# Performance work log

Measured on AMD Instinct MI355X. Metric: run time of the kernel, lower is better.

## Reference

```python
import jax, jax.numpy as jnp
import numpy as np

D_MODEL = 1024
N_HEADS = 16
HEAD_DIM = D_MODEL // N_HEADS
BATCH = 4
SEQ = 2048


def setup_inputs() -> dict:
    key = jax.random.key(0)
    ks = jax.random.split(key, 5)
    # Xavier uniform bound for square d_model x d_model weights
    bound = np.sqrt(6.0 / (D_MODEL + D_MODEL))
    x = jax.random.normal(ks[0], (BATCH, SEQ, D_MODEL), dtype=jnp.float32)
    attention_mask = jnp.ones((BATCH, SEQ), dtype=jnp.int32)
    wq = jax.random.uniform(ks[1], (D_MODEL, D_MODEL), jnp.float32, -bound, bound)
    wk = jax.random.uniform(ks[2], (D_MODEL, D_MODEL), jnp.float32, -bound, bound)
    wv = jax.random.uniform(ks[3], (D_MODEL, D_MODEL), jnp.float32, -bound, bound)
    wo = jax.random.uniform(ks[4], (D_MODEL, D_MODEL), jnp.float32, -bound, bound)
    return {"x": x, "attention_mask": attention_mask,
            "wq": wq, "wk": wk, "wv": wv, "wo": wo}


def reference(x, attention_mask, wq, wk, wv, wo):
    # x: (B, S, D). Linear weights stored torch-style (out, in): y = x @ W^T
    B, S, D = x.shape
    H, Hd = N_HEADS, HEAD_DIM
    scale = np.sqrt(Hd).astype(np.float32)

    def split_heads(t):  # (B,S,D) -> (B,H,S,Hd)
        return t.reshape(B, S, H, Hd).transpose(0, 2, 1, 3)

    q = split_heads(jnp.einsum('bsd,ed->bse', x, wq))
    k = split_heads(jnp.einsum('bsd,ed->bse', x, wk))
    v = split_heads(jnp.einsum('bsd,ed->bse', x, wv))

    scores = jnp.einsum('bhqd,bhkd->bhqk', q, k) / scale  # (B,H,S,S)

    causal = jnp.tril(jnp.ones((S, S), dtype=bool))  # True = keep
    keep = causal[None, None, :, :] & (attention_mask[:, None, None, :] != 0)
    scores = jnp.where(keep, scores, -jnp.inf)

    attn = jax.nn.softmax(scores, axis=-1)  # dropout: eval mode (identity)
    out = jnp.einsum('bhqk,bhkd->bhqd', attn, v)  # (B,H,S,Hd)
    out = out.transpose(0, 2, 1, 3).reshape(B, S, D)
    return jnp.einsum('bsd,ed->bse', out, wo)
```

## Files before the change

kernel.cpp:

```cpp
#include <hip/hip_runtime.h>
#include <cstdint>
#include <cstddef>

#define D_MODEL 1024
#define N_HEADS 16
#define HEAD_DIM 64
#define BATCH 4
#define SEQ 2048
#define M_TOTAL (BATCH * SEQ)

typedef __attribute__((ext_vector_type(8))) short bf16x8;
typedef __attribute__((ext_vector_type(4))) float f32x4;
typedef __attribute__((ext_vector_type(16))) float f32x16;

#define Q_SCALE 0.18033688011112042f

__device__ __forceinline__ unsigned short f2bu(float f) {
    union { float f; unsigned u; } x; x.f = f;
    unsigned r = x.u + 0x7FFFu + ((x.u >> 16) & 1u);
    return (unsigned short)(r >> 16);
}

__device__ __forceinline__ void async16(void* lds, const void* g) {
    __builtin_amdgcn_global_load_lds(
        (const __attribute__((address_space(1))) void*)g,
        (__attribute__((address_space(3))) void*)lds, 16, 0, 0);
}

__global__ __launch_bounds__(256) void cast_all(const float* __restrict__ x,
                                                const float* __restrict__ wq,
                                                const float* __restrict__ wk,
                                                const float* __restrict__ wv,
                                                const float* __restrict__ wo,
                                                unsigned short* __restrict__ dst) {
    const size_t NE = (size_t)M_TOTAL * D_MODEL;
    const size_t WE = (size_t)D_MODEL * D_MODEL;
    size_t i4 = (size_t)blockIdx.x * 256 + threadIdx.x;
    size_t e = i4 * 4;
    const float* src; size_t off;
    if (e < NE) { src = x; off = e; }
    else {
        size_t t = e - NE;
        int r = (int)(t / WE); off = t - (size_t)r * WE;
        src = (r == 0) ? wq : (r == 1) ? wk : (r == 2) ? wv : wo;
    }
    float4 v = *(const float4*)(src + off);
    ushort4 o;
    o.x = f2bu(v.x); o.y = f2bu(v.y); o.z = f2bu(v.z); o.w = f2bu(v.w);
    ((ushort4*)dst)[i4] = o;
}

__global__ __launch_bounds__(256) void qkv_gemm(const unsigned short* __restrict__ X,
                                                const unsigned short* __restrict__ W0,
                                                const unsigned short* __restrict__ W1,
                                                const unsigned short* __restrict__ W2,
                                                unsigned short* __restrict__ Y0,
                                                unsigned short* __restrict__ Y1,
                                                unsigned short* __restrict__ Vt) {
    __shared__ short As[2][128 * 32];
    __shared__ short Bs[2][128 * 32];

    const int id = (int)blockIdx.x + 24 * (int)blockIdx.y;
    const int xcd = id & 7, slot = id >> 3;
    const int ty = xcd * 8 + slot / 24;
    const int tx = slot % 24;

    const int sel = tx >> 3;
    const unsigned short* W = (sel == 0) ? W0 : (sel == 1) ? W1 : W2;
    const float scl = (sel == 0) ? Q_SCALE : 1.0f;

    const int tid = threadIdx.x;
    const int w = tid >> 6, lane = tid & 63, quad = lane >> 4, l15 = lane & 15;
    const int wm = w & 1, wn = w >> 1;
    const int rowBase = ty * 128;
    const int colBase = (tx & 7) * 128;

    int stRow[2], stCc[2];
#pragma unroll
    for (int l = 0; l < 2; ++l) {
        int c = tid + l * 256;
        stRow[l] = c >> 2;
        stCc[l] = (c & 3) ^ ((stRow[l] >> 1) & 3);
    }

    f32x4 acc[4][4];
#pragma unroll
    for (int mi = 0; mi < 4; ++mi)
#pragma unroll
        for (int ni = 0; ni < 4; ++ni)
#pragma unroll
            for (int e = 0; e < 4; ++e) acc[mi][ni][e] = 0.f;

#pragma unroll
    for (int l = 0; l < 2; ++l) {
        int c = tid + l * 256;
        async16((char*)As[0] + c * 16, X + (size_t)(rowBase + stRow[l]) * 1024 + stCc[l] * 8);
        async16((char*)Bs[0] + c * 16, W + (size_t)(colBase + stRow[l]) * 1024 + stCc[l] * 8);
    }
    __syncthreads();

    for (int kt = 0; kt < 32; ++kt) {
        const int buf = kt & 1;
        if (kt < 31) {
            const int kn = (kt + 1) * 32;
#pragma unroll
            for (int l = 0; l < 2; ++l) {
                int c = tid + l * 256;
                async16((char*)As[buf ^ 1] + c * 16,
                        X + (size_t)(rowBase + stRow[l]) * 1024 + kn + stCc[l] * 8);
                async16((char*)Bs[buf ^ 1] + c * 16,
                        W + (size_t)(colBase + stRow[l]) * 1024 + kn + stCc[l] * 8);
            }
        }

        bf16x8 a[4], b[4];
#pragma unroll
        for (int mi = 0; mi < 4; ++mi) {
            int r = wm * 64 + mi * 16 + l15;
            int slt = quad ^ ((r >> 1) & 3);
            a[mi] = *(const bf16x8*)&As[buf][r * 32 + slt * 8];
        }
#pragma unroll
        for (int ni = 0; ni < 4; ++ni) {
            int r = wn * 64 + ni * 16 + l15;
            int slt = quad ^ ((r >> 1) & 3);
            b[ni] = *(const bf16x8*)&Bs[buf][r * 32 + slt * 8];
        }
#pragma unroll
        for (int mi = 0; mi < 4; ++mi)
#pragma unroll
            for (int ni = 0; ni < 4; ++ni)
                acc[mi][ni] = __builtin_amdgcn_mfma_f32_16x16x32_bf16(a[mi], b[ni], acc[mi][ni], 0, 0, 0);

        __syncthreads();
    }

    if (sel != 2) {
        unsigned short* Y = (sel == 0) ? Y0 : Y1;
#pragma unroll
        for (int mi = 0; mi < 4; ++mi)
#pragma unroll
            for (int ni = 0; ni < 4; ++ni)
#pragma unroll
                for (int reg = 0; reg < 4; ++reg) {
                    int row = rowBase + wm * 64 + mi * 16 + quad * 4 + reg;
                    int col = colBase + wn * 64 + ni * 16 + l15;
                    Y[(size_t)row * 1024 + col] = f2bu(acc[mi][ni][reg] * scl);
                }
    } else {
#pragma unroll
        for (int mi = 0; mi < 4; ++mi) {
            int row0 = rowBase + wm * 64 + mi * 16 + quad * 4;
            int bb = row0 >> 11;
            int s0 = row0 & 2047;
#pragma unroll
            for (int ni = 0; ni < 4; ++ni) {
                int col = colBase + wn * 64 + ni * 16 + l15;
                int hh = col >> 6, dd = col & 63;
                ushort4 pk;
                pk.x = f2bu(acc[mi][ni][0]); pk.y = f2bu(acc[mi][ni][1]);
                pk.z = f2bu(acc[mi][ni][2]); pk.w = f2bu(acc[mi][ni][3]);
                *(ushort4*)(Vt + (((size_t)bb * 16 + hh) * 64 + dd) * SEQ + s0) = pk;
            }
        }
    }
}

__global__ __launch_bounds__(256) void out_gemm(const unsigned short* __restrict__ X,
                                                const unsigned short* __restrict__ W,
                                                float* __restrict__ Y) {
    __shared__ short As[2][128 * 32];
    __shared__ short Bs[2][128 * 32];

    const int id = (int)blockIdx.x + 8 * (int)blockIdx.y;
    const int xcd = id & 7, slot = id >> 3;
    const int ty = xcd * 8 + (slot >> 3);
    const int tx = slot & 7;

    const int tid = threadIdx.x;
    const int w = tid >> 6, lane = tid & 63, quad = lane >> 4, l15 = lane & 15;
    const int wm = w & 1, wn = w >> 1;
    const int rowBase = ty * 128;
    const int colBase = tx * 128;

    int stRow[2], stCc[2];
#pragma unroll
    for (int l = 0; l < 2; ++l) {
        int c = tid + l * 256;
        stRow[l] = c >> 2;
        stCc[l] = (c & 3) ^ ((stRow[l] >> 1) & 3);
    }

    f32x4 acc[4][4];
#pragma unroll
    for (int mi = 0; mi < 4; ++mi)
#pragma unroll
        for (int ni = 0; ni < 4; ++ni)
#pragma unroll
            for (int e = 0; e < 4; ++e) acc[mi][ni][e] = 0.f;

#pragma unroll
    for (int l = 0; l < 2; ++l) {
        int c = tid + l * 256;
        async16((char*)As[0] + c * 16, X + (size_t)(rowBase + stRow[l]) * 1024 + stCc[l] * 8);
        async16((char*)Bs[0] + c * 16, W + (size_t)(colBase + stRow[l]) * 1024 + stCc[l] * 8);
    }
    __syncthreads();

    for (int kt = 0; kt < 32; ++kt) {
        const int buf = kt & 1;
        if (kt < 31) {
            const int kn = (kt + 1) * 32;
#pragma unroll
            for (int l = 0; l < 2; ++l) {
                int c = tid + l * 256;
                async16((char*)As[buf ^ 1] + c * 16,
                        X + (size_t)(rowBase + stRow[l]) * 1024 + kn + stCc[l] * 8);
                async16((char*)Bs[buf ^ 1] + c * 16,
                        W + (size_t)(colBase + stRow[l]) * 1024 + kn + stCc[l] * 8);
            }
        }

        bf16x8 a[4], b[4];
#pragma unroll
        for (int mi = 0; mi < 4; ++mi) {
            int r = wm * 64 + mi * 16 + l15;
            int slt = quad ^ ((r >> 1) & 3);
            a[mi] = *(const bf16x8*)&As[buf][r * 32 + slt * 8];
        }
#pragma unroll
        for (int ni = 0; ni < 4; ++ni) {
            int r = wn * 64 + ni * 16 + l15;
            int slt = quad ^ ((r >> 1) & 3);
            b[ni] = *(const bf16x8*)&Bs[buf][r * 32 + slt * 8];
        }
#pragma unroll
        for (int mi = 0; mi < 4; ++mi)
#pragma unroll
            for (int ni = 0; ni < 4; ++ni)
                acc[mi][ni] = __builtin_amdgcn_mfma_f32_16x16x32_bf16(a[mi], b[ni], acc[mi][ni], 0, 0, 0);

        __syncthreads();
    }

#pragma unroll
    for (int mi = 0; mi < 4; ++mi)
#pragma unroll
        for (int ni = 0; ni < 4; ++ni)
#pragma unroll
            for (int reg = 0; reg < 4; ++reg) {
                int row = rowBase + wm * 64 + mi * 16 + quad * 4 + reg;
                int col = colBase + wn * 64 + ni * 16 + l15;
                Y[(size_t)row * 1024 + col] = acc[mi][ni][reg];
            }
}

__global__ __launch_bounds__(256) void flash32(const unsigned short* __restrict__ Q,
                                               const unsigned short* __restrict__ K,
                                               const unsigned short* __restrict__ Vt,
                                               const int* __restrict__ mask,
                                               unsigned short* __restrict__ CTX) {
    __shared__ short lds[16384];
    __shared__ float biasS[2][64];
    __shared__ int allokS[2];
    __shared__ int okW[4];

    const int bh = blockIdx.x;
    const int pid = blockIdx.y;
    const int b = bh >> 4;
    const int tid = threadIdx.x;
    const int w = tid >> 6, lane = tid & 63, l31 = lane & 31, lane5 = lane >> 5;

    const size_t qkBase = (size_t)b * SEQ * D_MODEL + (size_t)(bh & 15) * HEAD_DIM;
    const size_t vtBase = (size_t)bh * HEAD_DIM * SEQ;

    {
        int ok = 1;
        for (int i = tid; i < SEQ; i += 256) ok &= (mask[b * SEQ + i] != 0);
        unsigned long long bal = __ballot(ok != 0);
        if (lane == 0) okW[w] = (bal == ~0ull) ? 1 : 0;
    }
    __syncthreads();
    const int allSeq = okW[0] & okW[1] & okW[2] & okW[3];

    int stp[2], stcc[2], stj[2];
#pragma unroll
    for (int l = 0; l < 2; ++l) {
        int c = tid + l * 256;
        int p = c >> 3, sl = c & 7;
        stp[l] = p;
        stcc[l] = sl ^ (p & 7);
        stj[l] = (p & 0x33) | ((p & 4) << 1) | ((p & 8) >> 1);
    }

    for (int phase = 0; phase < 2; ++phase) {
        const int qt = phase ? pid : 15 - pid;
        const int q0 = qt * 128;
        const int iq = q0 + w * 32 + l31;

        bf16x8 qf[4];
#pragma unroll
        for (int ks = 0; ks < 4; ++ks)
            qf[ks] = *(const bf16x8*)(Q + qkBase + (size_t)iq * D_MODEL + ks * 16 + lane5 * 8);

        float mv = -INFINITY, lv = 0.f;
        f32x16 Ot[2];
#pragma unroll
        for (int dt = 0; dt < 2; ++dt)
#pragma unroll
            for (int e = 0; e < 16; ++e) Ot[dt][e] = 0.f;

        const int ktmax = 2 * qt + 1;

        uint4 kreg[2], vreg[2];
        int mreg = 1;
#pragma unroll
        for (int l = 0; l < 2; ++l) {
            kreg[l] = *(const uint4*)(K + qkBase + (size_t)stj[l] * D_MODEL + stcc[l] * 8);
            vreg[l] = *(const uint4*)(Vt + vtBase + (size_t)stp[l] * SEQ + stcc[l] * 8);
        }
        if (!allSeq && tid < 64) mreg = mask[b * SEQ + tid];

        for (int kt = 0; kt <= ktmax; ++kt) {
            const int k0 = kt * 64;
            const int buf = kt & 1;
#pragma unroll
            for (int l = 0; l < 2; ++l) {
                int c = tid + l * 256;
                *(uint4*)((char*)lds + buf * 8192 + c * 16) = kreg[l];
                *(uint4*)((char*)lds + 16384 + buf * 8192 + c * 16) = vreg[l];
            }
            if (!allSeq && tid < 64) {
                biasS[buf][tid] = mreg ? 0.f : -INFINITY;
                unsigned long long bal = __ballot(mreg != 0);
                if (tid == 0) allokS[buf] = (bal == ~0ull) ? 1 : 0;
            }
            if (kt < ktmax) {
                const int kn = k0 + 64;
#pragma unroll
                for (int l = 0; l < 2; ++l) {
                    kreg[l] = *(const uint4*)(K + qkBase + (size_t)(kn + stj[l]) * D_MODEL + stcc[l] * 8);
                    vreg[l] = *(const uint4*)(Vt + vtBase + (size_t)stp[l] * SEQ + kn + stcc[l] * 8);
                }
                if (!allSeq && tid < 64) mreg = mask[b * SEQ + kn + tid];
            }
            __syncthreads();

            if (64 * kt > q0 + 32 * w + 31) continue;

            const short* Ks = lds + buf * 4096;
            const short* Vs = lds + 8192 + buf * 4096;

            const int kHi = q0 + 32 * w + 31 - k0;
            const int nT = (kHi >= 32) ? 2 : 1;
            const int nt = ((kHi >> 4) >= 3 ? 3 : (kHi >> 4)) + 1;

            f32x16 St[2];
            __builtin_amdgcn_s_setprio(1);
#pragma unroll
            for (int T = 0; T < 2; ++T) {
                if (T < nT) {
#pragma unroll
                    for (int e = 0; e < 16; ++e) St[T][e] = 0.f;
#pragma unroll
                    for (int ks = 0; ks < 4; ++ks) {
                        int p = T * 32 + l31;
                        int slot = (ks * 2 + lane5) ^ (p & 7);
                        bf16x8 a = *(const bf16x8*)&Ks[p * 64 + slot * 8];
                        St[T] = __builtin_amdgcn_mfma_f32_32x32x16_bf16(a, qf[ks], St[T], 0, 0, 0);
                    }
                }
            }
            __builtin_amdgcn_s_setprio(0);

            const bool partial = (k0 + 63 > q0 + 32 * w);
            if (partial) {
#pragma unroll
                for (int T = 0; T < 2; ++T)
                    if (T < nT)
#pragma unroll
                        for (int r = 0; r < 16; ++r) {
                            int j = k0 + 32 * T + 16 * (r >> 3) + 8 * lane5 + (r & 7);
                            if (j > iq) St[T][r] = -INFINITY;
                        }
            }
            if (!allSeq && !allokS[buf]) {
#pragma unroll
                for (int T = 0; T < 2; ++T)
                    if (T < nT)
#pragma unroll
                        for (int r = 0; r < 16; ++r)
                            St[T][r] += biasS[buf][32 * T + 16 * (r >> 3) + 8 * lane5 + (r & 7)];
            }

            float tm[2];
#pragma unroll
            for (int T = 0; T < 2; ++T) {
                if (T < nT) {
                    float a0 = fmaxf(fmaxf(St[T][0], St[T][1]), fmaxf(St[T][2], St[T][3]));
                    float a1 = fmaxf(fmaxf(St[T][4], St[T][5]), fmaxf(St[T][6], St[T][7]));
                    float a2 = fmaxf(fmaxf(St[T][8], St[T][9]), fmaxf(St[T][10], St[T][11]));
                    float a3 = fmaxf(fmaxf(St[T][12], St[T][13]), fmaxf(St[T][14], St[T][15]));
                    tm[T] = fmaxf(fmaxf(a0, a1), fmaxf(a2, a3));
                } else tm[T] = -INFINITY;
            }
            float rm = fmaxf(tm[0], tm[1]);
            rm = fmaxf(rm, __shfl_xor(rm, 32));
            float mn = fmaxf(mv, rm);
            if (mn > mv + 8.f) {
                float al = exp2f(mv - mn);
                lv *= al;
#pragma unroll
                for (int dt = 0; dt < 2; ++dt)
#pragma unroll
                    for (int e = 0; e < 16; ++e) Ot[dt][e] *= al;
                mv = mn;
            }
            float rsp[2] = {0.f, 0.f};
#pragma unroll
            for (int T = 0; T < 2; ++T) {
                if (T < nT) {
#pragma unroll
                    for (int r = 0; r < 16; ++r) {
                        float pv = exp2f(St[T][r] - mv);
                        St[T][r] = pv;
                        rsp[T] += pv;
                    }
                }
            }
            float rs = rsp[0] + rsp[1];
            rs += __shfl_xor(rs, 32);
            lv += rs;

            bf16x8 pf[4];
#pragma unroll
            for (int t = 0; t < 4; ++t) {
                if (t < nt) {
                    const int T = t >> 1, hb = t & 1;
                    unsigned u0, u1, u2, u3;
                    asm("v_cvt_pk_bf16_f32 %0, %1, %2" : "=v"(u0)
                        : "v"(St[T][hb * 8 + 0]), "v"(St[T][hb * 8 + 1]));
                    asm("v_cvt_pk_bf16_f32 %0, %1, %2" : "=v"(u1)
                        : "v"(St[T][hb * 8 + 2]), "v"(St[T][hb * 8 + 3]));
                    asm("v_cvt_pk_bf16_f32 %0, %1, %2" : "=v"(u2)
                        : "v"(St[T][hb * 8 + 4]), "v"(St[T][hb * 8 + 5]));
                    asm("v_cvt_pk_bf16_f32 %0, %1, %2" : "=v"(u3)
                        : "v"(St[T][hb * 8 + 6]), "v"(St[T][hb * 8 + 7]));
                    union { unsigned u[4]; bf16x8 v; } pk;
                    pk.u[0] = u0; pk.u[1] = u1; pk.u[2] = u2; pk.u[3] = u3;
                    pf[t] = pk.v;
                }
            }

            __builtin_amdgcn_s_setprio(1);
#pragma unroll
            for (int dt = 0; dt < 2; ++dt)
#pragma unroll
                for (int t = 0; t < 4; ++t) {
                    if (t < nt) {
                        int p = dt * 32 + l31;
                        int slot = (t * 2 + lane5) ^ (p & 7);
                        bf16x8 a = *(const bf16x8*)&Vs[p * 64 + slot * 8];
                        Ot[dt] = __builtin_amdgcn_mfma_f32_32x32x16_bf16(a, pf[t], Ot[dt], 0, 0, 0);
                    }
                }
            __builtin_amdgcn_s_setprio(0);
        }

        __syncthreads();
        const float inv = 1.f / lv;
#pragma unroll
        for (int dt = 0; dt < 2; ++dt)
#pragma unroll
            for (int k = 0; k < 8; ++k) {
                int r0 = 2 * k;
                int d = (r0 & 3) + 4 * lane5 + 8 * (r0 >> 2) + 32 * dt;
                unsigned lo = f2bu(Ot[dt][r0] * inv);
                unsigned hi = f2bu(Ot[dt][r0 + 1] * inv);
                *(unsigned*)&lds[(w * 32 + l31) * 72 + d] = lo | (hi << 16);
            }
        __syncthreads();
#pragma unroll
        for (int k = 0; k < 4; ++k) {
            int id = tid + k * 256;
            int r = id >> 3, cc = id & 7;
            uint4 v = *(const uint4*)&lds[r * 72 + cc * 8];
            *(uint4*)(CTX + qkBase + (size_t)(q0 + r) * D_MODEL + cc * 8) = v;
        }
        __syncthreads();
    }
}

extern "C" void kernel_launch(void* const* d_in, const int* in_sizes, int n_in,
                              void* d_out, int out_size, void* d_ws, size_t ws_size,
                              hipStream_t stream) {
    const float* x  = (const float*)d_in[0];
    const int* mask = (const int*)d_in[1];
    const float* wq = (const float*)d_in[2];
    const float* wk = (const float*)d_in[3];
    const float* wv = (const float*)d_in[4];
    const float* wo = (const float*)d_in[5];
    float* out = (float*)d_out;

    const size_t NE = (size_t)M_TOTAL * D_MODEL;
    const size_t WE = (size_t)D_MODEL * D_MODEL;
    unsigned short* ws  = (unsigned short*)d_ws;
    unsigned short* xb  = ws;
    unsigned short* wqb = xb + NE;
    unsigned short* wkb = wqb + WE;
    unsigned short* wvb = wkb + WE;
    unsigned short* wob = wvb + WE;
    unsigned short* Qb  = wob + WE;
    unsigned short* Kb  = Qb + NE;
    unsigned short* Vtb = Kb + NE;
    unsigned short* CTX = Vtb + NE;

    cast_all<<<(int)((NE + 4 * WE) / 4 / 256), 256, 0, stream>>>(x, wq, wk, wv, wo, ws);

    qkv_gemm<<<dim3(24, M_TOTAL / 128), 256, 0, stream>>>(xb, wqb, wkb, wvb, Qb, Kb, Vtb);

    flash32<<<dim3(64, 8), 256, 0, stream>>>(Qb, Kb, Vtb, mask, CTX);

    out_gemm<<<dim3(D_MODEL / 128, M_TOTAL / 128), 256, 0, stream>>>(CTX, wob, out);
}
```

Before: 307.3 us.

## Fuse fp32-to-bf16 casts into GEMM tile loads, drop separate cast kernel

Removes the standalone cast_all kernel. The QKV and output GEMMs now read fp32 operands directly into registers, convert them with packed bf16 conversion instructions, and store them to LDS after the MFMA step. This cuts one launch and the write and re-read of the bf16 copies. In exchange the GEMMs read twice the bytes per tile, are re-read many times across tiles, and lose the async direct-to-LDS loads, which adds register pressure and VALU work inside the main loop.

New measurement: 340.0 us. +10.6%, slower.

```diff
diff --git a/kernel.cpp b/kernel.cpp
--- a/kernel.cpp
+++ b/kernel.cpp
@@ -27,33 +27,20 @@
         (__attribute__((address_space(3))) void*)lds, 16, 0, 0);
 }
 
-__global__ __launch_bounds__(256) void cast_all(const float* __restrict__ x,
-                                                const float* __restrict__ wq,
-                                                const float* __restrict__ wk,
-                                                const float* __restrict__ wv,
-                                                const float* __restrict__ wo,
-                                                unsigned short* __restrict__ dst) {
-    const size_t NE = (size_t)M_TOTAL * D_MODEL;
-    const size_t WE = (size_t)D_MODEL * D_MODEL;
-    size_t i4 = (size_t)blockIdx.x * 256 + threadIdx.x;
-    size_t e = i4 * 4;
-    const float* src; size_t off;
-    if (e < NE) { src = x; off = e; }
-    else {
-        size_t t = e - NE;
-        int r = (int)(t / WE); off = t - (size_t)r * WE;
-        src = (r == 0) ? wq : (r == 1) ? wk : (r == 2) ? wv : wo;
-    }
-    float4 v = *(const float4*)(src + off);
-    ushort4 o;
-    o.x = f2bu(v.x); o.y = f2bu(v.y); o.z = f2bu(v.z); o.w = f2bu(v.w);
-    ((ushort4*)dst)[i4] = o;
-}
-
-__global__ __launch_bounds__(256) void qkv_gemm(const unsigned short* __restrict__ X,
-                                                const unsigned short* __restrict__ W0,
-                                                const unsigned short* __restrict__ W1,
-                                                const unsigned short* __restrict__ W2,
+__device__ __forceinline__ uint4 cvt8(float4 a, float4 b) {
+    unsigned u0, u1, u2, u3;
+    asm("v_cvt_pk_bf16_f32 %0, %1, %2" : "=v"(u0) : "v"(a.x), "v"(a.y));
+    asm("v_cvt_pk_bf16_f32 %0, %1, %2" : "=v"(u1) : "v"(a.z), "v"(a.w));
+    asm("v_cvt_pk_bf16_f32 %0, %1, %2" : "=v"(u2) : "v"(b.x), "v"(b.y));
+    asm("v_cvt_pk_bf16_f32 %0, %1, %2" : "=v"(u3) : "v"(b.z), "v"(b.w));
+    uint4 r; r.x = u0; r.y = u1; r.z = u2; r.w = u3;
+    return r;
+}
+
+__global__ __launch_bounds__(256) void qkv_gemm(const float* __restrict__ X,
+                                                const float* __restrict__ W0,
+                                                const float* __restrict__ W1,
+                                                const float* __restrict__ W2,
                                                 unsigned short* __restrict__ Y0,
                                                 unsigned short* __restrict__ Y1,
                                                 unsigned short* __restrict__ Vt) {
@@ -66,7 +53,7 @@
     const int tx = slot % 24;
 
     const int sel = tx >> 3;
-    const unsigned short* W = (sel == 0) ? W0 : (sel == 1) ? W1 : W2;
+    const float* W = (sel == 0) ? W0 : (sel == 1) ? W1 : W2;
     const float scl = (sel == 0) ? Q_SCALE : 1.0f;
 
     const int tid = threadIdx.x;
@@ -91,11 +78,19 @@
 #pragma unroll
             for (int e = 0; e < 4; ++e) acc[mi][ni][e] = 0.f;
 
+    float4 ar[2][2], br[2][2];
+#pragma unroll
+    for (int l = 0; l < 2; ++l) {
+        const float* pa = X + (size_t)(rowBase + stRow[l]) * 1024 + stCc[l] * 8;
+        const float* pb = W + (size_t)(colBase + stRow[l]) * 1024 + stCc[l] * 8;
+        ar[l][0] = *(const float4*)pa; ar[l][1] = *(const float4*)(pa + 4);
+        br[l][0] = *(const float4*)pb; br[l][1] = *(const float4*)(pb + 4);
+    }
 #pragma unroll
     for (int l = 0; l < 2; ++l) {
         int c = tid + l * 256;
-        async16((char*)As[0] + c * 16, X + (size_t)(rowBase + stRow[l]) * 1024 + stCc[l] * 8);
-        async16((char*)Bs[0] + c * 16, W + (size_t)(colBase + stRow[l]) * 1024 + stCc[l] * 8);
+        *(uint4*)((char*)As[0] + c * 16) = cvt8(ar[l][0], ar[l][1]);
+        *(uint4*)((char*)Bs[0] + c * 16) = cvt8(br[l][0], br[l][1]);
     }
     __syncthreads();
 
@@ -105,11 +100,10 @@
             const int kn = (kt + 1) * 32;
 #pragma unroll
             for (int l = 0; l < 2; ++l) {
-                int c = tid + l * 256;
-                async16((char*)As[buf ^ 1] + c * 16,
-                        X + (size_t)(rowBase + stRow[l]) * 1024 + kn + stCc[l] * 8);
-                async16((char*)Bs[buf ^ 1] + c * 16,
-                        W + (size_t)(colBase + stRow[l]) * 1024 + kn + stCc[l] * 8);
+                const float* pa = X + (size_t)(rowBase + stRow[l]) * 1024 + kn + stCc[l] * 8;
+                const float* pb = W + (size_t)(colBase + stRow[l]) * 1024 + kn + stCc[l] * 8;
+                ar[l][0] = *(const float4*)pa; ar[l][1] = *(const float4*)(pa + 4);
+                br[l][0] = *(const float4*)pb; br[l][1] = *(const float4*)(pb + 4);
             }
         }
 
@@ -132,6 +126,14 @@
             for (int ni = 0; ni < 4; ++ni)
                 acc[mi][ni] = __builtin_amdgcn_mfma_f32_16x16x32_bf16(a[mi], b[ni], acc[mi][ni], 0, 0, 0);
 
+        if (kt < 31) {
+#pragma unroll
+            for (int l = 0; l < 2; ++l) {
+                int c = tid + l * 256;
+                *(uint4*)((char*)As[buf ^ 1] + c * 16) = cvt8(ar[l][0], ar[l][1]);
+                *(uint4*)((char*)Bs[buf ^ 1] + c * 16) = cvt8(br[l][0], br[l][1]);
+            }
+        }
         __syncthreads();
     }
 
@@ -167,7 +169,7 @@
 }
 
 __global__ __launch_bounds__(256) void out_gemm(const unsigned short* __restrict__ X,
-                                                const unsigned short* __restrict__ W,
+                                                const float* __restrict__ W,
                                                 float* __restrict__ Y) {
     __shared__ short As[2][128 * 32];
     __shared__ short Bs[2][128 * 32];
@@ -199,11 +201,18 @@
 #pragma unroll
             for (int e = 0; e < 4; ++e) acc[mi][ni][e] = 0.f;
 
+    float4 br[2][2];
 #pragma unroll
     for (int l = 0; l < 2; ++l) {
         int c = tid + l * 256;
         async16((char*)As[0] + c * 16, X + (size_t)(rowBase + stRow[l]) * 1024 + stCc[l] * 8);
-        async16((char*)Bs[0] + c * 16, W + (size_t)(colBase + stRow[l]) * 1024 + stCc[l] * 8);
+        const float* pb = W + (size_t)(colBase + stRow[l]) * 1024 + stCc[l] * 8;
+        br[l][0] = *(const float4*)pb; br[l][1] = *(const float4*)(pb + 4);
+    }
+#pragma unroll
+    for (int l = 0; l < 2; ++l) {
+        int c = tid + l * 256;
+        *(uint4*)((char*)Bs[0] + c * 16) = cvt8(br[l][0], br[l][1]);
     }
     __syncthreads();
 
@@ -216,8 +225,8 @@
                 int c = tid + l * 256;
                 async16((char*)As[buf ^ 1] + c * 16,
                         X + (size_t)(rowBase + stRow[l]) * 1024 + kn + stCc[l] * 8);
-                async16((char*)Bs[buf ^ 1] + c * 16,
-                        W + (size_t)(colBase + stRow[l]) * 1024 + kn + stCc[l] * 8);
+                const float* pb = W + (size_t)(colBase + stRow[l]) * 1024 + kn + stCc[l] * 8;
+                br[l][0] = *(const float4*)pb; br[l][1] = *(const float4*)(pb + 4);
             }
         }
 
@@ -240,6 +249,13 @@
             for (int ni = 0; ni < 4; ++ni)
                 acc[mi][ni] = __builtin_amdgcn_mfma_f32_16x16x32_bf16(a[mi], b[ni], acc[mi][ni], 0, 0, 0);
 
+        if (kt < 31) {
+#pragma unroll
+            for (int l = 0; l < 2; ++l) {
+                int c = tid + l * 256;
+                *(uint4*)((char*)Bs[buf ^ 1] + c * 16) = cvt8(br[l][0], br[l][1]);
+            }
+        }
         __syncthreads();
     }
 
@@ -503,23 +519,15 @@
     float* out = (float*)d_out;
 
     const size_t NE = (size_t)M_TOTAL * D_MODEL;
-    const size_t WE = (size_t)D_MODEL * D_MODEL;
     unsigned short* ws  = (unsigned short*)d_ws;
-    unsigned short* xb  = ws;
-    unsigned short* wqb = xb + NE;
-    unsigned short* wkb = wqb + WE;
-    unsigned short* wvb = wkb + WE;
-    unsigned short* wob = wvb + WE;
-    unsigned short* Qb  = wob + WE;
+    unsigned short* Qb  = ws;
     unsigned short* Kb  = Qb + NE;
     unsigned short* Vtb = Kb + NE;
     unsigned short* CTX = Vtb + NE;
 
-    cast_all<<<(int)((NE + 4 * WE) / 4 / 256), 256, 0, stream>>>(x, wq, wk, wv, wo, ws);
-
-    qkv_gemm<<<dim3(24, M_TOTAL / 128), 256, 0, stream>>>(xb, wqb, wkb, wvb, Qb, Kb, Vtb);
+    qkv_gemm<<<dim3(24, M_TOTAL / 128), 256, 0, stream>>>(x, wq, wk, wv, Qb, Kb, Vtb);
 
     flash32<<<dim3(64, 8), 256, 0, stream>>>(Qb, Kb, Vtb, mask, CTX);
 
-    out_gemm<<<dim3(D_MODEL / 128, M_TOTAL / 128), 256, 0, stream>>>(CTX, wob, out);
-}
+    out_gemm<<<dim3(D_MODEL / 128, M_TOTAL / 128), 256, 0, stream>>>(CTX, wo, out);
+}
```
